# Kernel optimization log

Hardware: AMD Instinct MI355X
Metric: run time of the kernel (lower is better)

The kernel has to match this reference:

```python
import jax, jax.numpy as jnp
import numpy as np
import math

B, N, D, H = 2, 64, 256, 8
DK = D // H


def setup_inputs() -> dict:
    key = jax.random.key(0)
    ks = jax.random.split(key, 12)
    s = 1.0 / math.sqrt(D)
    inp = {
        "state": jax.random.normal(ks[0], (B, N, N, D), dtype=jnp.float32),
        "mask": jnp.zeros((B, N, N, N), dtype=bool),
        "W_lk": jax.random.normal(ks[1], (D, D), dtype=jnp.float32) * s,
        "b_lk": jnp.zeros((D,), dtype=jnp.float32),
        "W_rk": jax.random.normal(ks[2], (D, D), dtype=jnp.float32) * s,
        "b_rk": jnp.zeros((D,), dtype=jnp.float32),
        "W_lv": jax.random.normal(ks[3], (D, D), dtype=jnp.float32) * s,
        "b_lv": jnp.zeros((D,), dtype=jnp.float32),
        "W_rv": jax.random.normal(ks[4], (D, D), dtype=jnp.float32) * s,
        "b_rv": jnp.zeros((D,), dtype=jnp.float32),
        "W_o": jax.random.normal(ks[5], (D, D), dtype=jnp.float32) * s,
        "b_o": jnp.zeros((D,), dtype=jnp.float32),
    }
    return inp


def _proj(x, W, b):
    # torch nn.Linear: x @ W.T + b, then view to heads
    y = jnp.einsum('bxyd,ed->bxye', x, W) + b
    return y.reshape(B, N, N, H, DK)


def reference(state, mask, W_lk, b_lk, W_rk, b_rk, W_lv, b_lv, W_rv, b_rv, W_o, b_o):
    left_k = _proj(state, W_lk, b_lk)   # [B,N,N,H,DK]
    right_k = _proj(state, W_rk, b_rk)
    left_v = _proj(state, W_lv, b_lv)
    right_v = _proj(state, W_rv, b_rv)

    # triangle-style scores over node triples (x, a, y): [B,N,N,N,H]
    scores = jnp.einsum('bxahd,bayhd->bxayh', left_k, right_k) / math.sqrt(DK)
    scores = jnp.where(mask[..., None], jnp.float32(-1000.0), scores)
    att = jax.nn.softmax(scores, axis=2)  # softmax over intermediate node a

    # val[b,x,a,y,h,d] = left_v[b,x,a,h,d] * right_v[b,a,y,h,d] (materialized as in torch)
    val = jnp.einsum('bxahd,bayhd->bxayhd', left_v, right_v)
    x = jnp.einsum('bxayh,bxayhd->bxyhd', att, val)  # sum over a
    x = x.reshape(B, N, N, D)
    return jnp.einsum('bxyd,ed->bxye', x, W_o) + b_o
```

## Files before the change

kernel.cpp:

```cpp
#include <hip/hip_runtime.h>

#define B 2
#define N 64
#define D 256
#define H 8
#define DK 32
#define M (B * N * N)

typedef __attribute__((ext_vector_type(8))) short bf16x8;
typedef __attribute__((ext_vector_type(4))) float f32x4;

#define OFF_LK 0
#define OFF_RK 256
#define OFF_LV 512
#define OFF_RV 768

__device__ __forceinline__ ushort f2b(float f) {
    union { float f; unsigned u; } v; v.f = f;
    unsigned r = v.u + 0x7fffu + ((v.u >> 16) & 1u);
    return (ushort)(r >> 16);
}
__device__ __forceinline__ float b2f(ushort u) {
    union { unsigned u; float f; } v; v.u = ((unsigned)u) << 16; return v.f;
}
__device__ __forceinline__ void cvt8(float4 raw, float* f) {
    const ushort* s = (const ushort*)&raw;
#pragma unroll
    for (int j = 0; j < 8; ++j) f[j] = b2f(s[j]);
}

__device__ __forceinline__ void glds16(const ushort* g, ushort* l) {
    __builtin_amdgcn_global_load_lds(
        (const __attribute__((address_space(1))) unsigned int*)g,
        (__attribute__((address_space(3))) unsigned int*)l, 16, 0, 0);
}

__global__ __launch_bounds__(256) void cast_all(const float* __restrict__ state,
                                                const float* __restrict__ W_lk, const float* __restrict__ W_rk,
                                                const float* __restrict__ W_lv, const float* __restrict__ W_rv,
                                                const float* __restrict__ W_o,
                                                const float* __restrict__ b_lk, const float* __restrict__ b_rk,
                                                const float* __restrict__ b_lv, const float* __restrict__ b_rv,
                                                const float* __restrict__ b_o,
                                                ushort* __restrict__ state_bf,
                                                ushort* __restrict__ Wcat,
                                                float* __restrict__ bias_cat) {
    const int gid = blockIdx.x * 256 + threadIdx.x;
    const float* Ws[5] = {W_lk, W_rk, W_lv, W_rv, W_o};
    const float* bs[5] = {b_lk, b_rk, b_lv, b_rv, b_o};

    if (gid < 1280) bias_cat[gid] = bs[gid >> 8][gid & 255];

    if (gid < 524288) {
        float4 v = *(const float4*)&state[(size_t)gid * 4];
        ushort4 o = {f2b(v.x), f2b(v.y), f2b(v.z), f2b(v.w)};
        *(ushort4*)&state_bf[(size_t)gid * 4] = o;
    } else {
        int u = gid - 524288;
        int row = u >> 6;
        int k4 = (u & 63) * 4;
        const float* W = Ws[row >> 8];
        float4 v = *(const float4*)&W[(size_t)(row & 255) * 256 + k4];
        ushort4 o = {f2b(v.x), f2b(v.y), f2b(v.z), f2b(v.w)};
        *(ushort4*)&Wcat[(size_t)row * 256 + k4] = o;
    }
}

template <int BF16OUT>
__global__ __launch_bounds__(256) void gemm_mfma(const ushort* __restrict__ A,
                                                 const ushort* __restrict__ Bw,
                                                 const float* __restrict__ bias,
                                                 void* __restrict__ Cv, int ldc) {
    __shared__ __align__(16) ushort As[128 * 32];
    __shared__ __align__(16) ushort Bs[128 * 32];
    const int tid = threadIdx.x;
    const int lane = tid & 63;
    const int wave = tid >> 6;
    const int wm = (wave & 1) * 64;
    const int wn = (wave >> 1) * 64;
    const int row0 = blockIdx.x * 128;
    const int col0 = blockIdx.y * 128;

    const int lr = lane >> 2;
    const int lkq = (lane & 3) * 8;

    const ushort* gA0 = A + (size_t)(row0 + wave * 32 + lr) * 256 + lkq;
    const ushort* gA1 = gA0 + 16 * 256;
    const ushort* gB0 = Bw + (size_t)(col0 + wave * 32 + lr) * 256 + lkq;
    const ushort* gB1 = gB0 + 16 * 256;
    ushort* lA0 = &As[(wave * 32) * 32];
    ushort* lA1 = &As[(wave * 32 + 16) * 32];
    ushort* lB0 = &Bs[(wave * 32) * 32];
    ushort* lB1 = &Bs[(wave * 32 + 16) * 32];

    const int fr = lane & 15;
    const int fk = (lane >> 4) * 8;

    f32x4 acc[4][4] = {};

    for (int k0 = 0; k0 < 256; k0 += 32) {
        __syncthreads();
        glds16(gA0 + k0, lA0);
        glds16(gA1 + k0, lA1);
        glds16(gB0 + k0, lB0);
        glds16(gB1 + k0, lB1);
        __syncthreads();

        bf16x8 af[4], bf[4];
#pragma unroll
        for (int i = 0; i < 4; ++i)
            af[i] = *(const bf16x8*)&As[(wm + i * 16 + fr) * 32 + fk];
#pragma unroll
        for (int j = 0; j < 4; ++j)
            bf[j] = *(const bf16x8*)&Bs[(wn + j * 16 + fr) * 32 + fk];
#pragma unroll
        for (int i = 0; i < 4; ++i)
#pragma unroll
            for (int j = 0; j < 4; ++j)
                acc[i][j] = __builtin_amdgcn_mfma_f32_16x16x32_bf16(af[i], bf[j], acc[i][j], 0, 0, 0);
    }

#pragma unroll
    for (int j = 0; j < 4; ++j) {
        const int col = col0 + wn + j * 16 + (lane & 15);
        const float bv = bias[col];
#pragma unroll
        for (int i = 0; i < 4; ++i) {
            const int rbase = row0 + wm + i * 16 + (lane >> 4) * 4;
#pragma unroll
            for (int r = 0; r < 4; ++r) {
                float o = acc[i][j][r] + bv;
                if (BF16OUT) ((ushort*)Cv)[(size_t)(rbase + r) * ldc + col] = f2b(o);
                else ((float*)Cv)[(size_t)(rbase + r) * ldc + col] = o;
            }
        }
    }
}

__global__ __launch_bounds__(512) void fused_attn(const ushort* __restrict__ P,
                                                  const unsigned char* __restrict__ mask,
                                                  ushort* __restrict__ xbuf) {
    __shared__ __align__(16) ushort LKs[16 * 16 * 32];
    __shared__ __align__(16) ushort RKs[16 * 16 * 32];
    __shared__ __align__(16) float LVs[16 * 16 * 44];
    __shared__ __align__(16) float RVs[16 * 16 * 44];
    __shared__ __align__(16) float atts[16 * 16 * 20];
    __shared__ __align__(16) unsigned char masks[16 * 16 * 16];
    __shared__ float mstate[16 * 20];
    __shared__ float lstate[16 * 20];
    __shared__ float alphas[16 * 20];

    const int bh = blockIdx.z;
    const int b = bh >> 3, h = bh & 7;
    const int x0 = blockIdx.x * 16, y0 = blockIdx.y * 16;
    const int tid = threadIdx.x;
    const int lane = tid & 63, wave = tid >> 6;

    const int y2 = (tid >> 4) & 3, dp = tid & 15;
    const int sx = tid >> 4, sy = tid & 15;
    if (tid < 256) {
        mstate[sx * 20 + sy] = -3.0e38f;
        lstate[sx * 20 + sy] = 0.0f;
    }

    float2 acc[2][4] = {};
    const float scale = 0.17677669529663687f;

    for (int ac = 0; ac < N; ac += 16) {
        __syncthreads();
        {
            const int xl = lane >> 2;
            const int qb = (lane & 3) * 8;
#pragma unroll
            for (int aw = 0; aw < 2; ++aw) {
                const int a = wave * 2 + aw;
                glds16(&P[(((size_t)b * N + x0 + xl) * N + ac + a) * 1024 + OFF_LK + h * DK + qb],
                       &LKs[a * 16 * 32]);
                glds16(&P[(((size_t)b * N + ac + a) * N + y0 + xl) * 1024 + OFF_RK + h * DK + qb],
                       &RKs[a * 16 * 32]);
            }
#pragma unroll
            for (int it = 0; it < 2; ++it) {
                const int row = (tid >> 2) + it * 128;
                const int q = tid & 3;
                const int a = row >> 4, r = row & 15;
                float f[8];
                cvt8(*(const float4*)&P[(((size_t)b * N + x0 + r) * N + ac + a) * 1024 + OFF_LV + h * DK + q * 8], f);
                *(float4*)&LVs[row * 44 + q * 8]     = make_float4(f[0], f[1], f[2], f[3]);
                *(float4*)&LVs[row * 44 + q * 8 + 4] = make_float4(f[4], f[5], f[6], f[7]);
                cvt8(*(const float4*)&P[(((size_t)b * N + ac + a) * N + y0 + r) * 1024 + OFF_RV + h * DK + q * 8], f);
                *(float4*)&RVs[row * 44 + q * 8]     = make_float4(f[0], f[1], f[2], f[3]);
                *(float4*)&RVs[row * 44 + q * 8 + 4] = make_float4(f[4], f[5], f[6], f[7]);
            }
            if (tid < 256) {
                const int xm = tid >> 4, am = tid & 15;
                *(int4*)&masks[(xm * 16 + am) * 16] =
                    *(const int4*)&mask[(((size_t)b * N + x0 + xm) * N + ac + am) * N + y0];
            }
        }
        __syncthreads();

        {
            const int fr = lane & 15, fk = (lane >> 4) * 8;
            const int yq = lane & 15, xq = (lane >> 4) * 4;
#pragma unroll
            for (int aw = 0; aw < 2; ++aw) {
                const int a = wave * 2 + aw;
                bf16x8 af = *(const bf16x8*)&LKs[(a * 16 + fr) * 32 + fk];
                bf16x8 bf = *(const bf16x8*)&RKs[(a * 16 + fr) * 32 + fk];
                f32x4 s = {};
                s = __builtin_amdgcn_mfma_f32_16x16x32_bf16(af, bf, s, 0, 0, 0);
#pragma unroll
                for (int rr = 0; rr < 4; ++rr) {
                    const int x = xq + rr;
                    float sv = s[rr] * scale;
                    if (masks[(x * 16 + a) * 16 + yq]) sv = -1000.0f;
                    atts[(a * 16 + x) * 20 + yq] = sv;
                }
            }
        }
        __syncthreads();

        if (tid < 256) {
            float s16[16];
            float mc = -3.0e38f;
#pragma unroll
            for (int a = 0; a < 16; ++a) {
                s16[a] = atts[(a * 16 + sx) * 20 + sy];
                mc = fmaxf(mc, s16[a]);
            }
            const float mold = mstate[sx * 20 + sy];
            const float mnew = fmaxf(mold, mc);
            const float alpha = __expf(mold - mnew);
            float ps = 0.0f;
#pragma unroll
            for (int a = 0; a < 16; ++a) {
                float p = __expf(s16[a] - mnew);
                atts[(a * 16 + sx) * 20 + sy] = p;
                ps += p;
            }
            lstate[sx * 20 + sy] = lstate[sx * 20 + sy] * alpha + ps;
            mstate[sx * 20 + sy] = mnew;
            alphas[sx * 20 + sy] = alpha;
        }
        __syncthreads();

#pragma unroll
        for (int i = 0; i < 2; ++i) {
            const int x = wave * 2 + i;
            float4 av = *(const float4*)&alphas[x * 20 + y2 * 4];
            const float* ap = (const float*)&av;
#pragma unroll
            for (int j = 0; j < 4; ++j) {
                acc[i][j].x *= ap[j];
                acc[i][j].y *= ap[j];
            }
        }
#pragma unroll
        for (int a = 0; a < 16; ++a) {
            float2 lv[2], rv[4];
#pragma unroll
            for (int i = 0; i < 2; ++i)
                lv[i] = *(const float2*)&LVs[(a * 16 + wave * 2 + i) * 44 + dp * 2];
#pragma unroll
            for (int j = 0; j < 4; ++j)
                rv[j] = *(const float2*)&RVs[(a * 16 + y2 * 4 + j) * 44 + dp * 2];
#pragma unroll
            for (int i = 0; i < 2; ++i) {
                float4 wv = *(const float4*)&atts[(a * 16 + wave * 2 + i) * 20 + y2 * 4];
                const float* wp = (const float*)&wv;
#pragma unroll
                for (int j = 0; j < 4; ++j) {
                    acc[i][j].x += (wp[j] * lv[i].x) * rv[j].x;
                    acc[i][j].y += (wp[j] * lv[i].y) * rv[j].y;
                }
            }
        }
    }

#pragma unroll
    for (int i = 0; i < 2; ++i) {
        const int x = wave * 2 + i;
        float4 lq = *(const float4*)&lstate[x * 20 + y2 * 4];
        const float* lp = (const float*)&lq;
#pragma unroll
        for (int j = 0; j < 4; ++j) {
            const float il = 1.0f / lp[j];
            ushort2 o = {f2b(acc[i][j].x * il), f2b(acc[i][j].y * il)};
            *(ushort2*)&xbuf[(((size_t)b * N + x0 + x) * N + y0 + y2 * 4 + j) * D + h * DK + 2 * dp] = o;
        }
    }
}

extern "C" void kernel_launch(void* const* d_in, const int* in_sizes, int n_in,
                              void* d_out, int out_size, void* d_ws, size_t ws_size,
                              hipStream_t stream) {
    const float* state = (const float*)d_in[0];
    const unsigned char* mask = (const unsigned char*)d_in[1];
    const float* W_lk = (const float*)d_in[2];
    const float* b_lk = (const float*)d_in[3];
    const float* W_rk = (const float*)d_in[4];
    const float* b_rk = (const float*)d_in[5];
    const float* W_lv = (const float*)d_in[6];
    const float* b_lv = (const float*)d_in[7];
    const float* W_rv = (const float*)d_in[8];
    const float* b_rv = (const float*)d_in[9];
    const float* W_o = (const float*)d_in[10];
    const float* b_o = (const float*)d_in[11];
    float* out = (float*)d_out;

    char* ws = (char*)d_ws;
    ushort* P_bf = (ushort*)ws;
    ws += (size_t)M * 1024 * 2;
    float* bias_cat = (float*)ws;
    ws += 1280 * 4;
    ushort* state_bf = (ushort*)ws;
    ws += (size_t)M * D * 2;
    ushort* Wcat = (ushort*)ws;
    ws += (size_t)1280 * 256 * 2;
    ushort* xbuf_bf = (ushort*)ws;

    cast_all<<<2368, 256, 0, stream>>>(state, W_lk, W_rk, W_lv, W_rv, W_o,
                                       b_lk, b_rk, b_lv, b_rv, b_o,
                                       state_bf, Wcat, bias_cat);
    gemm_mfma<1><<<dim3(M / 128, 8), 256, 0, stream>>>(state_bf, Wcat, bias_cat, P_bf, 1024);
    fused_attn<<<dim3(4, 4, B * H), 512, 0, stream>>>(P_bf, mask, xbuf_bf);
    gemm_mfma<0><<<dim3(M / 128, 2), 256, 0, stream>>>(xbuf_bf, Wcat + 1024 * 256, bias_cat + 1024, out, 256);
}
```

Baseline: 127.1 us.

## Store projections head-major and read K and mask directly from global memory

The projection GEMM now writes its output in a per-projection, per-(batch,head) contiguous layout instead of interleaved rows of 1024. The attention kernel drops the LDS staging of LK/RK and the mask, loading MFMA operands and mask bytes straight from global memory, which also removes one barrier per a-chunk. The goal is more contiguous reads and less LDS traffic and synchronisation. In exchange, the GEMM epilogue stores become scattered, and K and mask reads now depend on cache hits with smaller, less coalesced accesses.

Result: faster. 124.5 us (median of 2 runs) (-2.1%).

```diff
diff --git a/kernel.cpp b/kernel.cpp
--- a/kernel.cpp
+++ b/kernel.cpp
@@ -10,10 +10,7 @@
 typedef __attribute__((ext_vector_type(8))) short bf16x8;
 typedef __attribute__((ext_vector_type(4))) float f32x4;
 
-#define OFF_LK 0
-#define OFF_RK 256
-#define OFF_LV 512
-#define OFF_RV 768
+#define PROJ_ELEMS (2097152)
 
 __device__ __forceinline__ ushort f2b(float f) {
     union { float f; unsigned u; } v; v.f = f;
@@ -66,7 +63,7 @@
     }
 }
 
-template <int BF16OUT>
+template <int BF16OUT, int RELAYOUT>
 __global__ __launch_bounds__(256) void gemm_mfma(const ushort* __restrict__ A,
                                                  const ushort* __restrict__ Bw,
                                                  const float* __restrict__ bias,
@@ -130,8 +127,17 @@
 #pragma unroll
             for (int r = 0; r < 4; ++r) {
                 float o = acc[i][j][r] + bv;
-                if (BF16OUT) ((ushort*)Cv)[(size_t)(rbase + r) * ldc + col] = f2b(o);
-                else ((float*)Cv)[(size_t)(rbase + r) * ldc + col] = o;
+                if (RELAYOUT) {
+                    const int row = rbase + r;
+                    const int bb = row >> 12, rr = row & 4095;
+                    const int proj = col >> 8, hh = (col >> 5) & 7, dk = col & 31;
+                    ((ushort*)Cv)[(size_t)proj * PROJ_ELEMS +
+                                  ((size_t)(bb * 8 + hh) * 4096 + rr) * 32 + dk] = f2b(o);
+                } else if (BF16OUT) {
+                    ((ushort*)Cv)[(size_t)(rbase + r) * ldc + col] = f2b(o);
+                } else {
+                    ((float*)Cv)[(size_t)(rbase + r) * ldc + col] = o;
+                }
             }
         }
     }
@@ -140,12 +146,9 @@
 __global__ __launch_bounds__(512) void fused_attn(const ushort* __restrict__ P,
                                                   const unsigned char* __restrict__ mask,
                                                   ushort* __restrict__ xbuf) {
-    __shared__ __align__(16) ushort LKs[16 * 16 * 32];
-    __shared__ __align__(16) ushort RKs[16 * 16 * 32];
     __shared__ __align__(16) float LVs[16 * 16 * 44];
     __shared__ __align__(16) float RVs[16 * 16 * 44];
     __shared__ __align__(16) float atts[16 * 16 * 20];
-    __shared__ __align__(16) unsigned char masks[16 * 16 * 16];
     __shared__ float mstate[16 * 20];
     __shared__ float lstate[16 * 20];
     __shared__ float alphas[16 * 20];
@@ -156,6 +159,12 @@
     const int tid = threadIdx.x;
     const int lane = tid & 63, wave = tid >> 6;
 
+    const size_t HB = (size_t)bh * 4096 * 32;
+    const ushort* PLK = P + HB;
+    const ushort* PRK = P + (size_t)1 * PROJ_ELEMS + HB;
+    const ushort* PLV = P + (size_t)2 * PROJ_ELEMS + HB;
+    const ushort* PRV = P + (size_t)3 * PROJ_ELEMS + HB;
+
     const int y2 = (tid >> 4) & 3, dp = tid & 15;
     const int sx = tid >> 4, sy = tid & 15;
     if (tid < 256) {
@@ -168,53 +177,34 @@
 
     for (int ac = 0; ac < N; ac += 16) {
         __syncthreads();
-        {
-            const int xl = lane >> 2;
-            const int qb = (lane & 3) * 8;
-#pragma unroll
-            for (int aw = 0; aw < 2; ++aw) {
-                const int a = wave * 2 + aw;
-                glds16(&P[(((size_t)b * N + x0 + xl) * N + ac + a) * 1024 + OFF_LK + h * DK + qb],
-                       &LKs[a * 16 * 32]);
-                glds16(&P[(((size_t)b * N + ac + a) * N + y0 + xl) * 1024 + OFF_RK + h * DK + qb],
-                       &RKs[a * 16 * 32]);
-            }
-#pragma unroll
-            for (int it = 0; it < 2; ++it) {
-                const int row = (tid >> 2) + it * 128;
-                const int q = tid & 3;
-                const int a = row >> 4, r = row & 15;
-                float f[8];
-                cvt8(*(const float4*)&P[(((size_t)b * N + x0 + r) * N + ac + a) * 1024 + OFF_LV + h * DK + q * 8], f);
-                *(float4*)&LVs[row * 44 + q * 8]     = make_float4(f[0], f[1], f[2], f[3]);
-                *(float4*)&LVs[row * 44 + q * 8 + 4] = make_float4(f[4], f[5], f[6], f[7]);
-                cvt8(*(const float4*)&P[(((size_t)b * N + ac + a) * N + y0 + r) * 1024 + OFF_RV + h * DK + q * 8], f);
-                *(float4*)&RVs[row * 44 + q * 8]     = make_float4(f[0], f[1], f[2], f[3]);
-                *(float4*)&RVs[row * 44 + q * 8 + 4] = make_float4(f[4], f[5], f[6], f[7]);
-            }
-            if (tid < 256) {
-                const int xm = tid >> 4, am = tid & 15;
-                *(int4*)&masks[(xm * 16 + am) * 16] =
-                    *(const int4*)&mask[(((size_t)b * N + x0 + xm) * N + ac + am) * N + y0];
-            }
-        }
-        __syncthreads();
-
+#pragma unroll
+        for (int it = 0; it < 2; ++it) {
+            const int row = (tid >> 2) + it * 128;
+            const int q = tid & 3;
+            const int a = row >> 4, r = row & 15;
+            float f[8];
+            cvt8(*(const float4*)&PLV[((size_t)(x0 + r) * 64 + ac + a) * 32 + q * 8], f);
+            *(float4*)&LVs[row * 44 + q * 8]     = make_float4(f[0], f[1], f[2], f[3]);
+            *(float4*)&LVs[row * 44 + q * 8 + 4] = make_float4(f[4], f[5], f[6], f[7]);
+            cvt8(*(const float4*)&PRV[((size_t)(ac + a) * 64 + y0 + r) * 32 + q * 8], f);
+            *(float4*)&RVs[row * 44 + q * 8]     = make_float4(f[0], f[1], f[2], f[3]);
+            *(float4*)&RVs[row * 44 + q * 8 + 4] = make_float4(f[4], f[5], f[6], f[7]);
+        }
         {
             const int fr = lane & 15, fk = (lane >> 4) * 8;
             const int yq = lane & 15, xq = (lane >> 4) * 4;
 #pragma unroll
             for (int aw = 0; aw < 2; ++aw) {
                 const int a = wave * 2 + aw;
-                bf16x8 af = *(const bf16x8*)&LKs[(a * 16 + fr) * 32 + fk];
-                bf16x8 bf = *(const bf16x8*)&RKs[(a * 16 + fr) * 32 + fk];
+                bf16x8 af = *(const bf16x8*)&PLK[((size_t)(x0 + fr) * 64 + ac + a) * 32 + fk];
+                bf16x8 bf = *(const bf16x8*)&PRK[((size_t)(ac + a) * 64 + y0 + fr) * 32 + fk];
                 f32x4 s = {};
                 s = __builtin_amdgcn_mfma_f32_16x16x32_bf16(af, bf, s, 0, 0, 0);
 #pragma unroll
                 for (int rr = 0; rr < 4; ++rr) {
                     const int x = xq + rr;
                     float sv = s[rr] * scale;
-                    if (masks[(x * 16 + a) * 16 + yq]) sv = -1000.0f;
+                    if (mask[((size_t)(b * N + x0 + x) * N + ac + a) * N + y0 + yq]) sv = -1000.0f;
                     atts[(a * 16 + x) * 20 + yq] = sv;
                 }
             }
@@ -311,7 +301,7 @@
 
     char* ws = (char*)d_ws;
     ushort* P_bf = (ushort*)ws;
-    ws += (size_t)M * 1024 * 2;
+    ws += (size_t)4 * PROJ_ELEMS * 2;
     float* bias_cat = (float*)ws;
     ws += 1280 * 4;
     ushort* state_bf = (ushort*)ws;
@@ -323,7 +313,7 @@
     cast_all<<<2368, 256, 0, stream>>>(state, W_lk, W_rk, W_lv, W_rv, W_o,
                                        b_lk, b_rk, b_lv, b_rv, b_o,
                                        state_bf, Wcat, bias_cat);
-    gemm_mfma<1><<<dim3(M / 128, 8), 256, 0, stream>>>(state_bf, Wcat, bias_cat, P_bf, 1024);
+    gemm_mfma<1, 1><<<dim3(M / 128, 8), 256, 0, stream>>>(state_bf, Wcat, bias_cat, P_bf, 1024);
     fused_attn<<<dim3(4, 4, B * H), 512, 0, stream>>>(P_bf, mask, xbuf_bf);
-    gemm_mfma<0><<<dim3(M / 128, 2), 256, 0, stream>>>(xbuf_bf, Wcat + 1024 * 256, bias_cat + 1024, out, 256);
-}
+    gemm_mfma<0, 0><<<dim3(M / 128, 2), 256, 0, stream>>>(xbuf_bf, Wcat + 1024 * 256, bias_cat + 1024, out, 256);
+}
```
